# Optimization experiments

Hardware: AMD Instinct MI355X
Metric: run time of the kernel (lower is better)

Reference implementation:

```python
import jax, jax.numpy as jnp
import numpy as np

B, C, H, W = 4, 16, 512, 512


def setup_inputs() -> dict:
    key = jax.random.key(0)
    k1, k2, k3, k4, k5 = jax.random.split(key, 5)
    # positive depth in [0.5, 10.5] meters
    depth = jax.random.uniform(k1, (B, 1, H, W), dtype=jnp.float32) * 10.0 + 0.5
    # realistic, well-conditioned camera intrinsics per batch element
    fx = 500.0 + 20.0 * jax.random.normal(k2, (B,), dtype=jnp.float32)
    fy = 500.0 + 20.0 * jax.random.normal(k3, (B,), dtype=jnp.float32)
    zeros = jnp.zeros((B,), jnp.float32)
    ones = jnp.ones((B,), jnp.float32)
    K = jnp.stack([
        jnp.stack([fx, zeros, ones * (W / 2.0)], axis=-1),
        jnp.stack([zeros, fy, ones * (H / 2.0)], axis=-1),
        jnp.stack([zeros, zeros, ones], axis=-1),
    ], axis=1)  # [B,3,3]
    # near-identity rigid-ish transforms so homogeneous w ~ 1
    T = jnp.eye(4, dtype=jnp.float32)[None, None] + 0.05 * jax.random.normal(k4, (B, C, 4, 4), dtype=jnp.float32)
    masks = jax.random.randint(k5, (B, C, H, W), 0, 2).astype(jnp.bool_)
    return {"depth": depth, "K": K, "T": T, "masks": masks}


def reference(depth, K, T, masks):
    b, _, h, w = depth.shape
    c = masks.shape[1]
    n = h * w
    eps = 1e-10
    # --- depth -> point cloud ---
    u = jnp.arange(w, dtype=depth.dtype)
    v = jnp.arange(h, dtype=depth.dtype)
    uu, vv = jnp.meshgrid(u, v, indexing='xy')            # [H,W]
    uv1 = jnp.stack([uu, vv, jnp.ones_like(uu)], axis=-1)  # [H,W,3]
    K_inv = jnp.linalg.inv(K)                              # [B,3,3]
    d = jnp.transpose(depth, (0, 2, 3, 1))                 # [B,H,W,1]
    points_3d = jnp.einsum('bij,hwj->bhwi', K_inv, uv1) * d  # [B,H,W,3]
    # --- per-object masked transform (vectorized over all channels) ---
    pts = points_3d.reshape(b, n, 3)
    pts_h = jnp.concatenate([pts, jnp.ones((b, n, 1), pts.dtype)], axis=-1)  # [B,N,4]
    trans_h = jnp.einsum('bcij,bnj->bcni', T, pts_h)       # [B,C,N,4]
    trans3 = trans_h[..., :3] / (trans_h[..., 3:] + eps)   # [B,C,N,3]
    masks_flat = masks.reshape(b, c, n)
    out = pts
    for ci in range(c):
        out = jnp.where(masks_flat[:, ci, :, None], trans3[:, ci], out)
    tp = out.reshape(b, h, w, 3)                           # transformed points
    # --- reproject to depth map (scatter) ---
    p2h = jnp.einsum('bij,bhwj->bhwi', K, tp)              # [B,H,W,3]
    p2 = p2h[..., :2] / (p2h[..., 2:] + eps)
    Z = tp[..., 2]                                         # [B,H,W]
    u_idx = jnp.clip(p2[..., 0], 0, w - 1).astype(jnp.int32)
    v_idx = jnp.clip(p2[..., 1], 0, h - 1).astype(jnp.int32)
    b_idx = jnp.broadcast_to(jnp.arange(b)[:, None, None], (b, h, w))
    depth_map = depth.at[b_idx, 0, v_idx, u_idx].set(Z)
    return depth_map
```

## Files before the change

### kernel.cpp

```cpp
#include <hip/hip_runtime.h>
#include <stdint.h>

constexpr int B = 4, C = 16, H = 512, W = 512;
constexpr int N = H * W;
constexpr int BLOCKS_PER_BATCH = N / 256;
constexpr int NXCD = 8;
constexpr float EPS = 1e-10f;


__device__ __forceinline__ void swizzle_bn(int orig, int tid, int& b, int& n) {
    int xcd = orig & (NXCD - 1);
    int j   = orig >> 3;
    b       = j >> 7;
    int r   = j & 127;
    int blk = xcd * 128 + r;
    n = (blk << 8) + tid;
}

__global__ __launch_bounds__(256) void project_store_kernel(
    const float* __restrict__ depth,
    const float* __restrict__ K,
    const float* __restrict__ T,
    const int*   __restrict__ masks,
    unsigned long long* __restrict__ keys,
    unsigned long long* __restrict__ recs)
{
    __shared__ float Ts[16][17];

    int b, n;
    swizzle_bn(blockIdx.x, threadIdx.x, b, n);
    int idx = b * N + n;
    int v = n >> 9;
    int u = n & (W - 1);
    int lane = threadIdx.x & 63;

    {
        int t = threadIdx.x;
        int c = t >> 4, e = t & 15;
        Ts[e][c] = T[(size_t)b * 256 + t];
    }
    __syncthreads();

    float d = depth[idx];

    const float* Kb = K + b * 9;
    float k00 = Kb[0], k01 = Kb[1], k02 = Kb[2];
    float k10 = Kb[3], k11 = Kb[4], k12 = Kb[5];
    float k20 = Kb[6], k21 = Kb[7], k22 = Kb[8];

    float c00 =  (k11 * k22 - k12 * k21);
    float c01 = -(k10 * k22 - k12 * k20);
    float c02 =  (k10 * k21 - k11 * k20);
    float det = k00 * c00 + k01 * c01 + k02 * c02;
    float invdet = 1.0f / det;
    float i00 =  (k11 * k22 - k12 * k21) * invdet;
    float i01 = -(k01 * k22 - k02 * k21) * invdet;
    float i02 =  (k01 * k12 - k02 * k11) * invdet;
    float i10 = -(k10 * k22 - k12 * k20) * invdet;
    float i11 =  (k00 * k22 - k02 * k20) * invdet;
    float i12 = -(k00 * k12 - k02 * k10) * invdet;
    float i20 =  (k10 * k21 - k11 * k20) * invdet;
    float i21 = -(k00 * k21 - k01 * k20) * invdet;
    float i22 =  (k00 * k11 - k01 * k10) * invdet;

    float uf = (float)u, vf = (float)v;
    float px = (i00 * uf + i01 * vf + i02) * d;
    float py = (i10 * uf + i11 * vf + i12) * d;
    float pz = (i20 * uf + i21 * vf + i22) * d;

    const int* mb = masks + (size_t)b * C * N + n;
    int sel;
    {
        int m3 = mb[(size_t)15 * N], m2 = mb[(size_t)14 * N];
        int m1 = mb[(size_t)13 * N], m0 = mb[(size_t)12 * N];
        sel = m3 ? 15 : m2 ? 14 : m1 ? 13 : m0 ? 12 : -1;
        if (sel < 0) {
            m3 = mb[(size_t)11 * N]; m2 = mb[(size_t)10 * N];
            m1 = mb[(size_t)9 * N];  m0 = mb[(size_t)8 * N];
            sel = m3 ? 11 : m2 ? 10 : m1 ? 9 : m0 ? 8 : -1;
        }
        if (sel < 0) {
            m3 = mb[(size_t)7 * N]; m2 = mb[(size_t)6 * N];
            m1 = mb[(size_t)5 * N]; m0 = mb[(size_t)4 * N];
            sel = m3 ? 7 : m2 ? 6 : m1 ? 5 : m0 ? 4 : -1;
        }
        if (sel < 0) {
            m3 = mb[(size_t)3 * N]; m2 = mb[(size_t)2 * N];
            m1 = mb[(size_t)1 * N]; m0 = mb[0];
            sel = m3 ? 3 : m2 ? 2 : m1 ? 1 : m0 ? 0 : -1;
        }
    }

    float ox = px, oy = py, oz = pz;
    if (sel >= 0) {
        float tx = Ts[0][sel]  * px + Ts[1][sel]  * py + Ts[2][sel]  * pz + Ts[3][sel];
        float ty = Ts[4][sel]  * px + Ts[5][sel]  * py + Ts[6][sel]  * pz + Ts[7][sel];
        float tz = Ts[8][sel]  * px + Ts[9][sel]  * py + Ts[10][sel] * pz + Ts[11][sel];
        float tw = Ts[12][sel] * px + Ts[13][sel] * py + Ts[14][sel] * pz + Ts[15][sel];
        float denom = tw + EPS;
        ox = tx / denom;
        oy = ty / denom;
        oz = tz / denom;
    }

    float qx = k00 * ox + k01 * oy + k02 * oz;
    float qy = k10 * ox + k11 * oy + k12 * oz;
    float qz = k20 * ox + k21 * oy + k22 * oz;
    float zz = qz + EPS;
    float pu = qx / zz;
    float pv = qy / zz;
    pu = fminf(fmaxf(pu, 0.0f), (float)(W - 1));
    pv = fminf(fmaxf(pv, 0.0f), (float)(H - 1));
    int ui = (int)pu;
    int vi = (int)pv;
    unsigned t = (unsigned)(vi * W + ui);
    unsigned zbits = __float_as_uint(oz);

    recs[idx] = ((unsigned long long)t << 32) | (unsigned long long)zbits;

    bool dom = false;
    #pragma unroll
    for (int delta = 1; delta <= 4; ++delta) {
        unsigned tn = (unsigned)__shfl_down((int)t, delta);
        dom |= (lane + delta < 64) && (tn == t);
    }
    if (!dom) {
        keys[(size_t)b * N + t] =
            ((unsigned long long)(unsigned)n << 32) | (unsigned long long)zbits;
    }
}

__global__ __launch_bounds__(256) void fixup_kernel(
    unsigned long long* __restrict__ keys,
    const unsigned long long* __restrict__ recs)
{
    int b, n;
    swizzle_bn(blockIdx.x, threadIdx.x, b, n);
    int idx = b * N + n;
    int lane = threadIdx.x & 63;

    unsigned long long rec = recs[idx];
    unsigned t = (unsigned)(rec >> 32);
    unsigned zbits = (unsigned)rec;

    bool dom = false;
    #pragma unroll
    for (int delta = 1; delta <= 4; ++delta) {
        unsigned tn = (unsigned)__shfl_down((int)t, delta);
        dom |= (lane + delta < 64) && (tn == t);
    }
    if (dom) return;

    unsigned long long* cell = &keys[(size_t)b * N + t];
    unsigned hi = (unsigned)(*cell >> 32);
    if (hi > (unsigned)(N - 1) || hi < (unsigned)n) {
        unsigned long long key =
            ((unsigned long long)(unsigned)n << 32) | (unsigned long long)zbits;
        atomicMax(cell, key);
    }
}

__global__ __launch_bounds__(256) void resolve_kernel(
    const unsigned long long* __restrict__ keys,
    const float*              __restrict__ depth,
    float*                    __restrict__ out)
{
    int idx = blockIdx.x * blockDim.x + threadIdx.x;
    if (idx >= B * N) return;
    unsigned long long k = keys[idx];
    unsigned hi = (unsigned)(k >> 32);
    out[idx] = (hi <= (unsigned)(N - 1)) ? __uint_as_float((unsigned)k)
                                         : depth[idx];
}

extern "C" void kernel_launch(void* const* d_in, const int* in_sizes, int n_in,
                              void* d_out, int out_size, void* d_ws, size_t ws_size,
                              hipStream_t stream) {
    const float* depth = (const float*)d_in[0];
    const float* K     = (const float*)d_in[1];
    const float* T     = (const float*)d_in[2];
    const int*   masks = (const int*)d_in[3];
    float* out = (float*)d_out;

    char* ws = (char*)d_ws;
    unsigned long long* keys = (unsigned long long*)ws;
    unsigned long long* recs = (unsigned long long*)(ws + (size_t)B * N * 8);

    int grid = B * BLOCKS_PER_BATCH;
    project_store_kernel<<<grid, 256, 0, stream>>>(depth, K, T, masks, keys, recs);
    fixup_kernel<<<grid, 256, 0, stream>>>(keys, recs);
    resolve_kernel<<<grid, 256, 0, stream>>>(keys, depth, out);
}
```

Baseline: 132.2 us.

## Replace store+fixup passes with single 32-bit atomicMin pass and z-plane gather

Merges the projection-store and fixup kernels into one kernel that does an atomicMin on a 32-bit inverted source index per target pixel and writes each source's transformed Z to a separate plane. The resolve kernel then decodes the winning source index and gathers its Z. This drops one launch, the 64-bit record buffer round-trip and the 64-bit key traffic. In exchange it issues atomics for every non-dominated pixel and adds a random gather in resolve, and it depends on the workspace's initial key contents acting as a sentinel.

```diff
diff --git a/kernel.cpp b/kernel.cpp
--- a/kernel.cpp
+++ b/kernel.cpp
@@ -17,13 +17,13 @@
     n = (blk << 8) + tid;
 }
 
-__global__ __launch_bounds__(256) void project_store_kernel(
+__global__ __launch_bounds__(256) void project_atomic_kernel(
     const float* __restrict__ depth,
     const float* __restrict__ K,
     const float* __restrict__ T,
     const int*   __restrict__ masks,
-    unsigned long long* __restrict__ keys,
-    unsigned long long* __restrict__ recs)
+    unsigned*    __restrict__ keys,
+    float*       __restrict__ zplane)
 {
     __shared__ float Ts[16][17];
 
@@ -103,6 +103,8 @@
         oz = tz / denom;
     }
 
+    zplane[idx] = oz;
+
     float qx = k00 * ox + k01 * oy + k02 * oz;
     float qy = k10 * ox + k11 * oy + k12 * oz;
     float qz = k20 * ox + k21 * oy + k22 * oz;
@@ -114,9 +116,6 @@
     int ui = (int)pu;
     int vi = (int)pv;
     unsigned t = (unsigned)(vi * W + ui);
-    unsigned zbits = __float_as_uint(oz);
-
-    recs[idx] = ((unsigned long long)t << 32) | (unsigned long long)zbits;
 
     bool dom = false;
     #pragma unroll
@@ -125,52 +124,26 @@
         dom |= (lane + delta < 64) && (tn == t);
     }
     if (!dom) {
-        keys[(size_t)b * N + t] =
-            ((unsigned long long)(unsigned)n << 32) | (unsigned long long)zbits;
-    }
-}
-
-__global__ __launch_bounds__(256) void fixup_kernel(
-    unsigned long long* __restrict__ keys,
-    const unsigned long long* __restrict__ recs)
-{
-    int b, n;
-    swizzle_bn(blockIdx.x, threadIdx.x, b, n);
-    int idx = b * N + n;
-    int lane = threadIdx.x & 63;
-
-    unsigned long long rec = recs[idx];
-    unsigned t = (unsigned)(rec >> 32);
-    unsigned zbits = (unsigned)rec;
-
-    bool dom = false;
-    #pragma unroll
-    for (int delta = 1; delta <= 4; ++delta) {
-        unsigned tn = (unsigned)__shfl_down((int)t, delta);
-        dom |= (lane + delta < 64) && (tn == t);
-    }
-    if (dom) return;
-
-    unsigned long long* cell = &keys[(size_t)b * N + t];
-    unsigned hi = (unsigned)(*cell >> 32);
-    if (hi > (unsigned)(N - 1) || hi < (unsigned)n) {
-        unsigned long long key =
-            ((unsigned long long)(unsigned)n << 32) | (unsigned long long)zbits;
-        atomicMax(cell, key);
+        atomicMin(&keys[(size_t)b * N + t], (unsigned)(N - 1 - n));
     }
 }
 
 __global__ __launch_bounds__(256) void resolve_kernel(
-    const unsigned long long* __restrict__ keys,
-    const float*              __restrict__ depth,
-    float*                    __restrict__ out)
+    const unsigned* __restrict__ keys,
+    const float*    __restrict__ zplane,
+    const float*    __restrict__ depth,
+    float*          __restrict__ out)
 {
     int idx = blockIdx.x * blockDim.x + threadIdx.x;
     if (idx >= B * N) return;
-    unsigned long long k = keys[idx];
-    unsigned hi = (unsigned)(k >> 32);
-    out[idx] = (hi <= (unsigned)(N - 1)) ? __uint_as_float((unsigned)k)
-                                         : depth[idx];
+    int b = idx >> 18;
+    unsigned k = keys[idx];
+    if (k <= (unsigned)(N - 1)) {
+        int n_w = N - 1 - (int)k;
+        out[idx] = zplane[(size_t)b * N + n_w];
+    } else {
+        out[idx] = depth[idx];
+    }
 }
 
 extern "C" void kernel_launch(void* const* d_in, const int* in_sizes, int n_in,
@@ -183,11 +156,10 @@
     float* out = (float*)d_out;
 
     char* ws = (char*)d_ws;
-    unsigned long long* keys = (unsigned long long*)ws;
-    unsigned long long* recs = (unsigned long long*)(ws + (size_t)B * N * 8);
+    unsigned* keys  = (unsigned*)ws;
+    float* zplane   = (float*)(ws + (size_t)B * N * 4);
 
     int grid = B * BLOCKS_PER_BATCH;
-    project_store_kernel<<<grid, 256, 0, stream>>>(depth, K, T, masks, keys, recs);
-    fixup_kernel<<<grid, 256, 0, stream>>>(keys, recs);
-    resolve_kernel<<<grid, 256, 0, stream>>>(keys, depth, out);
+    project_atomic_kernel<<<grid, 256, 0, stream>>>(depth, K, T, masks, keys, zplane);
+    resolve_kernel<<<grid, 256, 0, stream>>>(keys, zplane, depth, out);
 }
```

After: 133.6 us. About the same (+1.1%).
